# Kernel optimization log

Measured on AMD Instinct MI355X. Metric: run time of the kernel, lower is better.

The kernel has to match this reference:

```python
import jax, jax.numpy as jnp
import numpy as np

N_HITS = 100_000
D_EMB = 12
N_OBJ = 1024          # object ids 1..N_OBJ, id 0 = noise (noise_threshold=0)
Q_MIN = 0.1
SB = 0.1
MAX_N_REP = 100_000
EPS = 1e-9


def setup_inputs() -> dict:
    key = jax.random.key(0)
    k1, k2, k3 = jax.random.split(key, 3)
    # beta in (0, 0.95) so arctanh stays finite (torch code asserts no NaN in q)
    beta = jax.random.uniform(k1, (N_HITS,), jnp.float32) * 0.95
    # scale embeddings so a realistic fraction of pairs has dist < 1 (repulsion active)
    x = jax.random.normal(k2, (N_HITS, D_EMB), jnp.float32) * 0.3
    object_id = jax.random.randint(k3, (N_HITS,), 0, N_OBJ + 1).astype(jnp.int64)
    return {"beta": beta, "x": x, "object_id": object_id}


def reference(beta, x, object_id):
    n = beta.shape[0]
    oids = jnp.arange(1, N_OBJ + 1)                      # [K] (all non-noise ids present w.h.p.)
    att = object_id[:, None] == oids[None, :]            # [N,K] attractive mask

    q = jnp.arctanh(beta) ** 2 + Q_MIN                   # [N] charge
    alphas = jnp.argmax(q[:, None] * att, axis=0)        # [K] condensation point per object
    x_a = x[alphas]                                      # [K,d]
    q_a = q[alphas]                                      # [K]

    # pairwise squared distances [N,K] (cdist)
    d2 = (jnp.sum(x * x, axis=1)[:, None]
          - 2.0 * (x @ x_a.T)
          + jnp.sum(x_a * x_a, axis=1)[None, :])
    d2 = jnp.maximum(d2, 0.0)
    dist = jnp.sqrt(jnp.maximum(d2, 1e-12))              # safe sqrt (grad-safe)

    qw = q[:, None] * q_a[None, :]                       # [N,K] q_j * q_alpha_k

    # attractive: mean over hits of q_j * sum_k M_jk * q_k * d^2  (use d2, not dist**2)
    v_att = jnp.sum(jnp.where(att, qw * d2, 0.0)) / n

    # repulsive hinge, capped via random subsampling with 1/freq upweighting
    rep = (~att) & (dist < 1.0)
    n_rep_k = jnp.sum(rep)
    freq = jnp.minimum(
        jnp.float32(MAX_N_REP) / jnp.maximum(n_rep_k, 1).astype(jnp.float32), 1.0)
    samp = jax.random.uniform(jax.random.key(42), dist.shape) < freq
    rep = rep & samp
    v_rep = jnp.sum(jnp.where(rep, qw * (1.0 - dist), 0.0)) / freq / n

    # coward: push condensation-point betas toward 1
    l_coward = jnp.mean(1.0 - beta[alphas])

    # noise: mean beta over noise hits (object_id <= noise_threshold=0)
    noise_mask = object_id <= 0
    l_noise = jnp.sum(jnp.where(noise_mask, beta, 0.0)) / (
        jnp.maximum(jnp.sum(noise_mask), 1).astype(beta.dtype) + EPS)

    loss = v_att + v_rep + l_coward + l_noise * SB
    return jnp.stack([v_att, v_rep, l_coward, l_noise, loss])
```

## Files before the change

### kernel.cpp

```cpp
#include <hip/hip_runtime.h>
#include <stdint.h>

#define NHITS 100000
#define NOBJ  1024
#define HALF  50000
#define QUART 25000
#define HALF_PAIRS 51200000u


#define MASK_OFF 873792ull
#define WS_NEED (MASK_OFF + 16ull * NHITS * 8ull)

__device__ inline uint32_t rotl32(uint32_t x, int n) {
    return (x << n) | (x >> (32 - n));
}

__device__ inline void threefry2x32(uint32_t k0, uint32_t k1,
                                    uint32_t x0, uint32_t x1,
                                    uint32_t& o0, uint32_t& o1) {
    uint32_t ks2 = k0 ^ k1 ^ 0x1BD11BDAu;
    x0 += k0; x1 += k1;
#define TF_ROUND(r) { x0 += x1; x1 = rotl32(x1, r); x1 ^= x0; }
    TF_ROUND(13) TF_ROUND(15) TF_ROUND(26) TF_ROUND(6)
    x0 += k1;  x1 += ks2 + 1u;
    TF_ROUND(17) TF_ROUND(29) TF_ROUND(16) TF_ROUND(24)
    x0 += ks2; x1 += k0 + 2u;
    TF_ROUND(13) TF_ROUND(15) TF_ROUND(26) TF_ROUND(6)
    x0 += k0;  x1 += k1 + 3u;
    TF_ROUND(17) TF_ROUND(29) TF_ROUND(16) TF_ROUND(24)
    x0 += k1;  x1 += ks2 + 4u;
    TF_ROUND(13) TF_ROUND(15) TF_ROUND(26) TF_ROUND(6)
    x0 += ks2; x1 += k0 + 5u;
#undef TF_ROUND
    o0 = x0; o1 = x1;
}

__device__ inline float tf_uniform(uint32_t bits) {
    return __uint_as_float((bits >> 9) | 0x3f800000u) - 1.0f;
}

__device__ inline float freq_from_n(unsigned int n) {
    if (n < 1u) n = 1u;
    return fminf(100000.0f / (float)n, 1.0f);
}

__device__ inline double waveReduceD(double v) {
    for (int off = 32; off > 0; off >>= 1) v += __shfl_down(v, off, 64);
    return v;
}
__device__ inline unsigned int waveReduceU(unsigned int v) {
    for (int off = 32; off > 0; off >>= 1) v += __shfl_down(v, off, 64);
    return v;
}

#define DOT12(XA, XB, XC, A, B, C) \
    fmaf((XC).w, (C).w, fmaf((XC).z, (C).z, fmaf((XC).y, (C).y, fmaf((XC).x, (C).x, \
    fmaf((XB).w, (B).w, fmaf((XB).z, (B).z, fmaf((XB).y, (B).y, fmaf((XB).x, (B).x, \
    fmaf((XA).w, (A).w, fmaf((XA).z, (A).z, fmaf((XA).y, (A).y, (XA).x * (A).x)))))))))))

#define SS12(XA, XB, XC) DOT12(XA, XB, XC, XA, XB, XC)


__global__ void k_init(unsigned long long* packed, unsigned long long* hdr) {
    int t = blockIdx.x * blockDim.x + threadIdx.x;
    if (t < NOBJ) packed[t] = 0xFFFFFFFFull;
    if (t < 8)    hdr[t] = 0ull;
}

__global__ void k_hits(const float* __restrict__ beta,
                       const float* __restrict__ x,
                       const int* __restrict__ oid,
                       unsigned long long* __restrict__ packed,
                       float* __restrict__ q_arr,
                       float* __restrict__ xx_arr,
                       double* __restrict__ noise_sum,
                       unsigned long long* __restrict__ noise_cnt) {
    int j = blockIdx.x * blockDim.x + threadIdx.x;
    float nb = 0.0f;
    unsigned int nc = 0;
    if (j < NHITS) {
        float b = beta[j];
        int o = oid[j];
        float a = atanhf(b);
        float q = a * a + 0.1f;
        q_arr[j] = q;
        const float4* x4 = (const float4*)x;
        float4 A = x4[j * 3 + 0], B = x4[j * 3 + 1], C = x4[j * 3 + 2];
        xx_arr[j] = SS12(A, B, C);
        if (o > 0) {
            unsigned long long p =
                ((unsigned long long)__float_as_uint(q) << 32) |
                (unsigned long long)(0xFFFFFFFFu - (unsigned)j);
            atomicMax(&packed[o - 1], p);
        } else {
            nb = b; nc = 1;
        }
    }
    double rb = waveReduceD((double)nb);
    unsigned int rc = waveReduceU(nc);
    if ((threadIdx.x & 63) == 0) {
        if (rb != 0.0) atomicAdd(noise_sum, rb);
        if (rc)        atomicAdd(noise_cnt, (unsigned long long)rc);
    }
}

__global__ void k_alphas(const unsigned long long* __restrict__ packed,
                         const float* __restrict__ x,
                         const float* __restrict__ beta,
                         const float* __restrict__ q_arr,
                         const float* __restrict__ xx_arr,
                         float* __restrict__ arec,
                         double* __restrict__ coward_sum) {
    int k = blockIdx.x * blockDim.x + threadIdx.x;
    double c = 0.0;
    if (k < NOBJ) {
        unsigned idx = 0xFFFFFFFFu - (unsigned)(packed[k] & 0xFFFFFFFFull);
        const float4* x4 = (const float4*)x;
        float4 A = x4[idx * 3 + 0];
        float4 B = x4[idx * 3 + 1];
        float4 C = x4[idx * 3 + 2];
        float4 D;
        D.x = q_arr[idx]; D.y = xx_arr[idx]; D.z = 0.f; D.w = 0.f;
        float4* ar = (float4*)arec;
        ar[k * 4 + 0] = A;
        ar[k * 4 + 1] = B;
        ar[k * 4 + 2] = C;
        ar[k * 4 + 3] = D;
        c = 1.0 - (double)beta[idx];
    }
    double rc = waveReduceD(c);
    if ((threadIdx.x & 63) == 0) atomicAdd(coward_sum, rc);
}

__global__ __launch_bounds__(256)
void k_scan(const float* __restrict__ x,
            const float* __restrict__ q_arr,
            const float* __restrict__ xx_arr,
            const int* __restrict__ oid,
            const float* __restrict__ arec,
            unsigned long long* __restrict__ mb64,
            unsigned int* __restrict__ nrep,
            double* __restrict__ v_att_sum,
            int do_write) {
    __shared__ float4 spack[64 * 4];
    __shared__ unsigned int su[4];
    __shared__ double sd[4];
    const int tid = threadIdx.x;
    const int kb = blockIdx.y * 64;
    const float4* ar4 = (const float4*)arec;
    spack[tid] = ar4[kb * 4 + tid];
    __syncthreads();

    const int t = blockIdx.x * 256 + tid;
    const bool valid = t < QUART;
    const int j0 = valid ? t : 0;
    const int j1 = j0 + QUART;
    const int j2 = j0 + 2 * QUART;
    const int j3 = j0 + 3 * QUART;
    const float4* x4 = (const float4*)x;

    float4 X0a = x4[j0 * 3 + 0], X0b = x4[j0 * 3 + 1], X0c = x4[j0 * 3 + 2];
    float4 X1a = x4[j1 * 3 + 0], X1b = x4[j1 * 3 + 1], X1c = x4[j1 * 3 + 2];
    float4 X2a = x4[j2 * 3 + 0], X2b = x4[j2 * 3 + 1], X2c = x4[j2 * 3 + 2];
    float4 X3a = x4[j3 * 3 + 0], X3b = x4[j3 * 3 + 1], X3c = x4[j3 * 3 + 2];

    const float inval = valid ? 0.0f : 3e9f;
    const float xx0 = xx_arr[j0] + inval;
    const float xx1 = xx_arr[j1] + inval;
    const float xx2 = xx_arr[j2] + inval;
    const float xx3 = xx_arr[j3] + inval;
    const int o0 = valid ? oid[j0] : 0;
    const int o1 = valid ? oid[j1] : 0;
    const int o2 = valid ? oid[j2] : 0;
    const int o3 = valid ? oid[j3] : 0;

    uint32_t mA0 = 0, mA1 = 0, mB0 = 0, mB1 = 0;
    uint32_t mC0 = 0, mC1 = 0, mD0 = 0, mD1 = 0;

#define SCANH(BASE, MA, MB, MC, MD)                                         \
    {                                                                       \
        uint32_t bit = 1u;                                                  \
        for (int kk = 0; kk < 32; ++kk, bit += bit) {                       \
            int kl = (BASE) + kk;                                           \
            float4 A = spack[kl * 4 + 0];                                   \
            float4 B = spack[kl * 4 + 1];                                   \
            float4 C = spack[kl * 4 + 2];                                   \
            float a2 = spack[kl * 4 + 3].y;                                 \
            float d0 = DOT12(X0a, X0b, X0c, A, B, C);                       \
            float d1 = DOT12(X1a, X1b, X1c, A, B, C);                       \
            float d2 = DOT12(X2a, X2b, X2c, A, B, C);                       \
            float d3 = DOT12(X3a, X3b, X3c, A, B, C);                       \
            float t0 = fmaf(-2.0f, d0, xx0) + a2;                           \
            float t1 = fmaf(-2.0f, d1, xx1) + a2;                           \
            float t2 = fmaf(-2.0f, d2, xx2) + a2;                           \
            float t3 = fmaf(-2.0f, d3, xx3) + a2;                           \
            MA |= (t0 < 1.0f) ? bit : 0u;                                   \
            MB |= (t1 < 1.0f) ? bit : 0u;                                   \
            MC |= (t2 < 1.0f) ? bit : 0u;                                   \
            MD |= (t3 < 1.0f) ? bit : 0u;                                   \
        }                                                                   \
    }
    SCANH(0,  mA0, mB0, mC0, mD0)
    SCANH(32, mA1, mB1, mC1, mD1)
#undef SCANH

    double vatt = 0.0;
#define ATT_SLOT(O, J, XA, XB, XC, XXV, LO, HI)                             \
    if ((O) > 0) {                                                          \
        int rel = (O) - 1 - kb;                                             \
        if (rel >= 0 && rel < 64) {                                         \
            uint32_t bb = ~(1u << (rel & 31));                              \
            if (rel < 32) LO &= bb; else HI &= bb;                          \
            float4 A = spack[rel * 4 + 0];                                  \
            float4 B = spack[rel * 4 + 1];                                  \
            float4 C = spack[rel * 4 + 2];                                  \
            float4 D = spack[rel * 4 + 3];                                  \
            float dot = DOT12(XA, XB, XC, A, B, C);                         \
            float d2r = fmaf(-2.0f, dot, XXV) + D.y;                        \
            vatt += (double)((q_arr[J] * D.x) * fmaxf(d2r, 0.0f));          \
        }                                                                   \
    }
    ATT_SLOT(o0, j0, X0a, X0b, X0c, xx0, mA0, mA1)
    ATT_SLOT(o1, j1, X1a, X1b, X1c, xx1, mB0, mB1)
    ATT_SLOT(o2, j2, X2a, X2b, X2c, xx2, mC0, mC1)
    ATT_SLOT(o3, j3, X3a, X3b, X3c, xx3, mD0, mD1)
#undef ATT_SLOT

    const unsigned long long M0 = (unsigned long long)mA0 | ((unsigned long long)mA1 << 32);
    const unsigned long long M1 = (unsigned long long)mB0 | ((unsigned long long)mB1 << 32);
    const unsigned long long M2 = (unsigned long long)mC0 | ((unsigned long long)mC1 << 32);
    const unsigned long long M3 = (unsigned long long)mD0 | ((unsigned long long)mD1 << 32);

    if (do_write && valid) {
        const size_t W = (size_t)blockIdx.y;
        mb64[W * NHITS + j0] = M0;
        mb64[W * NHITS + j1] = M1;
        mb64[W * NHITS + j2] = M2;
        mb64[W * NHITS + j3] = M3;
    }

    unsigned int cnt = (unsigned)(__popcll(M0) + __popcll(M1) +
                                  __popcll(M2) + __popcll(M3));
    unsigned int rc = waveReduceU(cnt);
    double rv = waveReduceD(vatt);
    if ((tid & 63) == 0) { su[tid >> 6] = rc; sd[tid >> 6] = rv; }
    __syncthreads();
    if (tid == 0) {
        unsigned int s = su[0] + su[1] + su[2] + su[3];
        if (s) atomicAdd(nrep, s);
        double v = sd[0] + sd[1] + sd[2] + sd[3];
        if (v != 0.0) atomicAdd(v_att_sum, v);
    }
}

__global__ __launch_bounds__(256)
void k_rep(const float* __restrict__ x,
           const float* __restrict__ q_arr,
           const float* __restrict__ xx_arr,
           const float* __restrict__ arec,
           const unsigned long long* __restrict__ mb64,
           const unsigned int* __restrict__ nrep,
           double* __restrict__ acc_out) {
    __shared__ unsigned short qq[4][4096];
    __shared__ double sd[4];
    const int tid = threadIdx.x;
    const int lane = tid & 63;
    const int w = tid >> 6;
    const int W = blockIdx.y;
    const int jblk = blockIdx.x * 1024;
    const float freq = freq_from_n(*nrep);
    const float4* x4 = (const float4*)x;
    const float4* ar = (const float4*)arec;
    double acc = 0.0;

    for (int r = 0; r < 4; ++r) {
        const int jround = jblk + r * 256 + (w << 6);
        const int j = jround + lane;
        unsigned long long m = (j < NHITS) ? mb64[(size_t)W * NHITS + j] : 0ull;
        unsigned int cnt = (unsigned)__popcll(m);

        unsigned int p = cnt;
#pragma unroll
        for (int off = 1; off < 64; off <<= 1) {
            unsigned int v = __shfl_up(p, off, 64);
            if (lane >= off) p += v;
        }
        const unsigned int excl = p - cnt;
        const unsigned int T = __shfl(p, 63, 64);

        {
            unsigned long long mm = m;
            unsigned int pos = excl;
            unsigned short base = (unsigned short)(lane << 6);
            while (mm) {
                int b = (int)__builtin_ctzll(mm);
                mm &= mm - 1ull;
                qq[w][pos++] = (unsigned short)(base | (unsigned short)b);
            }
        }
        __syncthreads();

        for (unsigned int i = lane; i < T; i += 64) {
            int desc = (int)qq[w][i];
            int jj = jround + (desc >> 6);
            int k = (W << 6) + (desc & 63);
            uint32_t f = (uint32_t)jj * NOBJ + (uint32_t)k;
            bool lo = jj < HALF;
            uint32_t xa = lo ? f : (f - HALF_PAIRS);
            uint32_t r0, r1;
            threefry2x32(0u, 42u, xa, xa + HALF_PAIRS, r0, r1);
            float u = tf_uniform(lo ? r0 : r1);
            if (u < freq) {
                float4 XA = x4[jj * 3 + 0], XB = x4[jj * 3 + 1], XC = x4[jj * 3 + 2];
                float4 A = ar[k * 4 + 0], B = ar[k * 4 + 1];
                float4 C = ar[k * 4 + 2], D = ar[k * 4 + 3];
                float dot = DOT12(XA, XB, XC, A, B, C);
                float d2 = fmaf(-2.0f, dot, xx_arr[jj]) + D.y;
                float dist = sqrtf(fmaxf(fmaxf(d2, 0.0f), 1e-12f));
                acc += (double)((q_arr[jj] * D.x) * (1.0f - dist));
            }
        }
        __syncthreads();
    }

    double rv = waveReduceD(acc);
    if (lane == 0) sd[w] = rv;
    __syncthreads();
    if (tid == 0) {
        double s = sd[0] + sd[1] + sd[2] + sd[3];
        if (s != 0.0) atomicAdd(acc_out, s);
    }
}

__global__ __launch_bounds__(256)
void k_rep_fb(const float* __restrict__ x,
              const float* __restrict__ q_arr,
              const float* __restrict__ xx_arr,
              const int* __restrict__ oid,
              const float* __restrict__ arec,
              const unsigned int* __restrict__ nrep,
              double* __restrict__ acc_out) {
    __shared__ double sacc[4];
    const int tid = threadIdx.x;
    int t = blockIdx.x * 256 + tid;
    bool valid = t < HALF;
    int j0 = valid ? t : 0;
    int j1 = j0 + HALF;
    const float4* x4 = (const float4*)x;
    float4 X0a = x4[j0 * 3 + 0], X0b = x4[j0 * 3 + 1], X0c = x4[j0 * 3 + 2];
    float4 X1a = x4[j1 * 3 + 0], X1b = x4[j1 * 3 + 1], X1c = x4[j1 * 3 + 2];
    float xx0 = valid ? xx_arr[j0] : 3e9f;
    float xx1 = valid ? xx_arr[j1] : 3e9f;
    int o0 = oid[j0], o1 = oid[j1];
    const float4* ar = (const float4*)arec;
    const int kb = blockIdx.y * 128;
    const float freq = freq_from_n(*nrep);

    double acc = 0.0;
#define FB_G(G, J, XA, XB, XC, XX, OO, S1)                                      \
    {                                                                           \
        uint32_t m = 0, bit = 1u;                                               \
        int kbase = kb + (G) * 32;                                              \
        for (int kk = 0; kk < 32; ++kk, bit += bit) {                           \
            int k = kbase + kk;                                                 \
            float4 A = ar[k * 4 + 0];                                           \
            float4 B = ar[k * 4 + 1];                                           \
            float4 C = ar[k * 4 + 2];                                           \
            float a2 = ar[k * 4 + 3].y;                                         \
            float d0 = DOT12(XA, XB, XC, A, B, C);                              \
            float t0 = fmaf(-2.0f, d0, XX) + a2;                                \
            m |= (t0 < 1.0f && (OO) != k + 1) ? bit : 0u;                       \
        }                                                                       \
        while (m) {                                                             \
            int kk = __ffs(m) - 1; m &= m - 1;                                  \
            int k = kbase + kk;                                                 \
            uint32_t f = (uint32_t)(J) * NOBJ + (uint32_t)k;                    \
            uint32_t xa_ = (S1) ? (f - HALF_PAIRS) : f;                         \
            uint32_t b0_, b1_;                                                  \
            threefry2x32(0u, 42u, xa_, xa_ + HALF_PAIRS, b0_, b1_);             \
            float u = tf_uniform((S1) ? b1_ : b0_);                             \
            if (u < freq) {                                                     \
                float4 A = ar[k * 4 + 0], B = ar[k * 4 + 1], C = ar[k * 4 + 2], D = ar[k * 4 + 3]; \
                float dot = DOT12(XA, XB, XC, A, B, C);                         \
                float d2 = fmaf(-2.0f, dot, XX) + D.y;                          \
                float dist = sqrtf(fmaxf(fmaxf(d2, 0.0f), 1e-12f));             \
                acc += (double)((q_arr[J] * D.x) * (1.0f - dist));              \
            }                                                                   \
        }                                                                       \
    }
    FB_G(0, j0, X0a, X0b, X0c, xx0, o0, false)
    FB_G(1, j0, X0a, X0b, X0c, xx0, o0, false)
    FB_G(2, j0, X0a, X0b, X0c, xx0, o0, false)
    FB_G(3, j0, X0a, X0b, X0c, xx0, o0, false)
    FB_G(0, j1, X1a, X1b, X1c, xx1, o1, true)
    FB_G(1, j1, X1a, X1b, X1c, xx1, o1, true)
    FB_G(2, j1, X1a, X1b, X1c, xx1, o1, true)
    FB_G(3, j1, X1a, X1b, X1c, xx1, o1, true)
#undef FB_G

    double rv = waveReduceD(acc);
    if ((tid & 63) == 0) sacc[tid >> 6] = rv;
    __syncthreads();
    if (tid == 0) {
        double s = sacc[0] + sacc[1] + sacc[2] + sacc[3];
        if (s != 0.0) atomicAdd(acc_out, s);
    }
}

__global__ void k_final(const double* __restrict__ accs,
                        const unsigned long long* __restrict__ noise_cnt,
                        const unsigned int* __restrict__ nrep,
                        float* __restrict__ out) {
    float freq = freq_from_n(*nrep);
    double v_att = accs[0] / (double)NHITS;
    double v_rep = accs[1] / (double)freq / (double)NHITS;
    double l_cow = accs[2] / (double)NOBJ;
    unsigned long long nc = *noise_cnt;
    if (nc < 1ull) nc = 1ull;
    double l_noise = accs[3] / ((double)nc + 1e-9);
    double loss = v_att + v_rep + l_cow + 0.1 * l_noise;
    out[0] = (float)v_att;
    out[1] = (float)v_rep;
    out[2] = (float)l_cow;
    out[3] = (float)l_noise;
    out[4] = (float)loss;
}


extern "C" void kernel_launch(void* const* d_in, const int* in_sizes, int n_in,
                              void* d_out, int out_size, void* d_ws, size_t ws_size,
                              hipStream_t stream) {
    const float* beta = (const float*)d_in[0];
    const float* x    = (const float*)d_in[1];
    const int*   oid  = (const int*)d_in[2];
    float* out = (float*)d_out;

    char* ws = (char*)d_ws;
    double* v_att_sum = (double*)(ws + 0);
    double* v_rep_sum = (double*)(ws + 8);
    double* coward_sum = (double*)(ws + 16);
    double* noise_sum = (double*)(ws + 24);
    unsigned long long* noise_cnt = (unsigned long long*)(ws + 32);
    unsigned int* nrep = (unsigned int*)(ws + 40);
    unsigned long long* packed = (unsigned long long*)(ws + 64);
    float* arec = (float*)(ws + 8256);
    float* q_arr = (float*)(ws + 73792);
    float* xx_arr = (float*)(ws + 473792);
    unsigned long long* mb64 = (unsigned long long*)(ws + MASK_OFF);

    const int wsok = (ws_size >= WS_NEED) ? 1 : 0;

    k_init<<<4, 256, 0, stream>>>(packed, (unsigned long long*)ws);
    k_hits<<<(NHITS + 255) / 256, 256, 0, stream>>>(beta, x, oid, packed,
                                                    q_arr, xx_arr,
                                                    noise_sum, noise_cnt);
    k_alphas<<<4, 256, 0, stream>>>(packed, x, beta, q_arr, xx_arr,
                                    arec, coward_sum);

    dim3 gs((QUART + 255) / 256, 16);
    k_scan<<<gs, 256, 0, stream>>>(x, q_arr, xx_arr, oid, arec,
                                   mb64, nrep, v_att_sum, wsok);

    if (wsok) {
        dim3 gr((NHITS + 1023) / 1024, 16);
        k_rep<<<gr, 256, 0, stream>>>(x, q_arr, xx_arr, arec, mb64,
                                      nrep, v_rep_sum);
    } else {
        dim3 gfb((HALF + 255) / 256, 8);
        k_rep_fb<<<gfb, 256, 0, stream>>>(x, q_arr, xx_arr, oid, arec,
                                          nrep, v_rep_sum);
    }

    k_final<<<1, 1, 0, stream>>>((double*)ws, noise_cnt, nrep, out);
}
```

Before: 131.8 us.

## Scan two hits per thread reading object records directly, folding attraction in-loop

The scan kernel now handles two hits per thread instead of four, which doubles the grid. It drops the shared-memory staging of the 64 object records and reads them straight from global memory, relying on uniform cached loads. The attractive term is computed inside the scan loop by matching the hit's own object index, instead of in a separate pass afterwards. Empty asm constraints pin the x registers, and the loop is partially unrolled. This trades reuse of each record load across four hits for more parallelism and fewer registers. It also adds a per-iteration compare and branch.

```diff
diff --git a/kernel.cpp b/kernel.cpp
--- a/kernel.cpp
+++ b/kernel.cpp
@@ -4,7 +4,6 @@
 #define NHITS 100000
 #define NOBJ  1024
 #define HALF  50000
-#define QUART 25000
 #define HALF_PAIRS 51200000u
 
 
@@ -142,105 +141,78 @@
             unsigned int* __restrict__ nrep,
             double* __restrict__ v_att_sum,
             int do_write) {
-    __shared__ float4 spack[64 * 4];
     __shared__ unsigned int su[4];
     __shared__ double sd[4];
     const int tid = threadIdx.x;
     const int kb = blockIdx.y * 64;
-    const float4* ar4 = (const float4*)arec;
-    spack[tid] = ar4[kb * 4 + tid];
-    __syncthreads();
 
     const int t = blockIdx.x * 256 + tid;
-    const bool valid = t < QUART;
+    const bool valid = t < HALF;
     const int j0 = valid ? t : 0;
-    const int j1 = j0 + QUART;
-    const int j2 = j0 + 2 * QUART;
-    const int j3 = j0 + 3 * QUART;
+    const int j1 = j0 + HALF;
     const float4* x4 = (const float4*)x;
 
-    float4 X0a = x4[j0 * 3 + 0], X0b = x4[j0 * 3 + 1], X0c = x4[j0 * 3 + 2];
-    float4 X1a = x4[j1 * 3 + 0], X1b = x4[j1 * 3 + 1], X1c = x4[j1 * 3 + 2];
-    float4 X2a = x4[j2 * 3 + 0], X2b = x4[j2 * 3 + 1], X2c = x4[j2 * 3 + 2];
-    float4 X3a = x4[j3 * 3 + 0], X3b = x4[j3 * 3 + 1], X3c = x4[j3 * 3 + 2];
+    float4 XAa = x4[j0 * 3 + 0], XAb = x4[j0 * 3 + 1], XAc = x4[j0 * 3 + 2];
+    float4 XBa = x4[j1 * 3 + 0], XBb = x4[j1 * 3 + 1], XBc = x4[j1 * 3 + 2];
+    asm volatile("" : "+v"(XAa.x), "+v"(XAa.y), "+v"(XAa.z), "+v"(XAa.w),
+                      "+v"(XAb.x), "+v"(XAb.y), "+v"(XAb.z), "+v"(XAb.w),
+                      "+v"(XAc.x), "+v"(XAc.y), "+v"(XAc.z), "+v"(XAc.w));
+    asm volatile("" : "+v"(XBa.x), "+v"(XBa.y), "+v"(XBa.z), "+v"(XBa.w),
+                      "+v"(XBb.x), "+v"(XBb.y), "+v"(XBb.z), "+v"(XBb.w),
+                      "+v"(XBc.x), "+v"(XBc.y), "+v"(XBc.z), "+v"(XBc.w));
 
     const float inval = valid ? 0.0f : 3e9f;
-    const float xx0 = xx_arr[j0] + inval;
-    const float xx1 = xx_arr[j1] + inval;
-    const float xx2 = xx_arr[j2] + inval;
-    const float xx3 = xx_arr[j3] + inval;
-    const int o0 = valid ? oid[j0] : 0;
-    const int o1 = valid ? oid[j1] : 0;
-    const int o2 = valid ? oid[j2] : 0;
-    const int o3 = valid ? oid[j3] : 0;
+    const float xxa = xx_arr[j0] + inval;
+    const float xxb = xx_arr[j1] + inval;
+    const int oa = valid ? oid[j0] : 0;
+    const int ob = valid ? oid[j1] : 0;
+    const int relA = (oa > 0) ? (oa - 1 - kb) : -1;
+    const int relB = (ob > 0) ? (ob - 1 - kb) : -1;
 
     uint32_t mA0 = 0, mA1 = 0, mB0 = 0, mB1 = 0;
-    uint32_t mC0 = 0, mC1 = 0, mD0 = 0, mD1 = 0;
-
-#define SCANH(BASE, MA, MB, MC, MD)                                         \
+    double vatt = 0.0;
+
+#define SCANH(BASE, MA, MB)                                                 \
     {                                                                       \
         uint32_t bit = 1u;                                                  \
+        _Pragma("unroll 8")                                                 \
         for (int kk = 0; kk < 32; ++kk, bit += bit) {                       \
-            int kl = (BASE) + kk;                                           \
-            float4 A = spack[kl * 4 + 0];                                   \
-            float4 B = spack[kl * 4 + 1];                                   \
-            float4 C = spack[kl * 4 + 2];                                   \
-            float a2 = spack[kl * 4 + 3].y;                                 \
-            float d0 = DOT12(X0a, X0b, X0c, A, B, C);                       \
-            float d1 = DOT12(X1a, X1b, X1c, A, B, C);                       \
-            float d2 = DOT12(X2a, X2b, X2c, A, B, C);                       \
-            float d3 = DOT12(X3a, X3b, X3c, A, B, C);                       \
-            float t0 = fmaf(-2.0f, d0, xx0) + a2;                           \
-            float t1 = fmaf(-2.0f, d1, xx1) + a2;                           \
-            float t2 = fmaf(-2.0f, d2, xx2) + a2;                           \
-            float t3 = fmaf(-2.0f, d3, xx3) + a2;                           \
-            MA |= (t0 < 1.0f) ? bit : 0u;                                   \
-            MB |= (t1 < 1.0f) ? bit : 0u;                                   \
-            MC |= (t2 < 1.0f) ? bit : 0u;                                   \
-            MD |= (t3 < 1.0f) ? bit : 0u;                                   \
+            const float* op = arec + (size_t)(kb + (BASE) + kk) * 16;       \
+            float4 A = *(const float4*)(op + 0);                            \
+            float4 B = *(const float4*)(op + 4);                            \
+            float4 C = *(const float4*)(op + 8);                            \
+            float qa_o = op[12];                                            \
+            float a2   = op[13];                                            \
+            float d0 = DOT12(XAa, XAb, XAc, A, B, C);                       \
+            float d1 = DOT12(XBa, XBb, XBc, A, B, C);                       \
+            float t0 = fmaf(-2.0f, d0, xxa) + a2;                           \
+            float t1 = fmaf(-2.0f, d1, xxb) + a2;                           \
+            const bool hA = ((BASE) + kk == relA);                          \
+            const bool hB = ((BASE) + kk == relB);                          \
+            MA |= (t0 < 1.0f && !hA) ? bit : 0u;                            \
+            MB |= (t1 < 1.0f && !hB) ? bit : 0u;                            \
+            if (hA || hB) {                                                 \
+                if (hA) vatt += (double)((q_arr[j0] * qa_o) * fmaxf(t0, 0.0f)); \
+                if (hB) vatt += (double)((q_arr[j1] * qa_o) * fmaxf(t1, 0.0f)); \
+            }                                                               \
         }                                                                   \
     }
-    SCANH(0,  mA0, mB0, mC0, mD0)
-    SCANH(32, mA1, mB1, mC1, mD1)
+    SCANH(0,  mA0, mB0)
+    SCANH(32, mA1, mB1)
 #undef SCANH
 
-    double vatt = 0.0;
-#define ATT_SLOT(O, J, XA, XB, XC, XXV, LO, HI)                             \
-    if ((O) > 0) {                                                          \
-        int rel = (O) - 1 - kb;                                             \
-        if (rel >= 0 && rel < 64) {                                         \
-            uint32_t bb = ~(1u << (rel & 31));                              \
-            if (rel < 32) LO &= bb; else HI &= bb;                          \
-            float4 A = spack[rel * 4 + 0];                                  \
-            float4 B = spack[rel * 4 + 1];                                  \
-            float4 C = spack[rel * 4 + 2];                                  \
-            float4 D = spack[rel * 4 + 3];                                  \
-            float dot = DOT12(XA, XB, XC, A, B, C);                         \
-            float d2r = fmaf(-2.0f, dot, XXV) + D.y;                        \
-            vatt += (double)((q_arr[J] * D.x) * fmaxf(d2r, 0.0f));          \
-        }                                                                   \
-    }
-    ATT_SLOT(o0, j0, X0a, X0b, X0c, xx0, mA0, mA1)
-    ATT_SLOT(o1, j1, X1a, X1b, X1c, xx1, mB0, mB1)
-    ATT_SLOT(o2, j2, X2a, X2b, X2c, xx2, mC0, mC1)
-    ATT_SLOT(o3, j3, X3a, X3b, X3c, xx3, mD0, mD1)
-#undef ATT_SLOT
-
-    const unsigned long long M0 = (unsigned long long)mA0 | ((unsigned long long)mA1 << 32);
-    const unsigned long long M1 = (unsigned long long)mB0 | ((unsigned long long)mB1 << 32);
-    const unsigned long long M2 = (unsigned long long)mC0 | ((unsigned long long)mC1 << 32);
-    const unsigned long long M3 = (unsigned long long)mD0 | ((unsigned long long)mD1 << 32);
+    const unsigned long long MA = (unsigned long long)mA0 |
+                                  ((unsigned long long)mA1 << 32);
+    const unsigned long long MB = (unsigned long long)mB0 |
+                                  ((unsigned long long)mB1 << 32);
 
     if (do_write && valid) {
         const size_t W = (size_t)blockIdx.y;
-        mb64[W * NHITS + j0] = M0;
-        mb64[W * NHITS + j1] = M1;
-        mb64[W * NHITS + j2] = M2;
-        mb64[W * NHITS + j3] = M3;
-    }
-
-    unsigned int cnt = (unsigned)(__popcll(M0) + __popcll(M1) +
-                                  __popcll(M2) + __popcll(M3));
+        mb64[W * NHITS + j0] = MA;
+        mb64[W * NHITS + j1] = MB;
+    }
+
+    unsigned int cnt = (unsigned)(__popcll(MA) + __popcll(MB));
     unsigned int rc = waveReduceU(cnt);
     double rv = waveReduceD(vatt);
     if ((tid & 63) == 0) { su[tid >> 6] = rc; sd[tid >> 6] = rv; }
@@ -457,7 +429,7 @@
     k_alphas<<<4, 256, 0, stream>>>(packed, x, beta, q_arr, xx_arr,
                                     arec, coward_sum);
 
-    dim3 gs((QUART + 255) / 256, 16);
+    dim3 gs((HALF + 255) / 256, 16);
     k_scan<<<gs, 256, 0, stream>>>(x, q_arr, xx_arr, oid, arec,
                                    mb64, nrep, v_att_sum, wsok);
 
```

Measured after the change: 170.5 us. 1.29x slower.
